# Kernel tuning notes

Hardware: AMD Instinct MI355X
Metric: run time of the kernel (lower is better)

## Reference

```python
import jax, jax.numpy as jnp
import numpy as np
from jax import lax

NPOINT = 1024
RADIUS = 0.2
NSAMPLE = 32
BN_EPS = 1e-5
MLP = [64, 64, 128]


def setup_inputs() -> dict:
    key = jax.random.key(0)
    ks = jax.random.split(key, 2 + 3 * len(MLP))
    B, N, D = 16, 4096, 64
    inp = {
        "xyz": jax.random.uniform(ks[0], (B, N, 3), dtype=jnp.float32),
        "points": jax.random.normal(ks[1], (B, N, D), dtype=jnp.float32),
    }
    last = 3 + D  # in_channel = 67
    for i, oc in enumerate(MLP):
        inp[f"w{i}"] = jax.random.normal(ks[2 + 3 * i], (oc, last), dtype=jnp.float32) / np.sqrt(last).astype(np.float32)
        inp[f"b{i}"] = jnp.zeros((oc,), jnp.float32)
        inp[f"g{i}"] = jnp.ones((oc,), jnp.float32)
        inp[f"bt{i}"] = jnp.zeros((oc,), jnp.float32)
        last = oc
    return inp


def _sqrdist(a, b):
    # ||a-b||^2 = |a|^2 + |b|^2 - 2 a.b   -> [B, S, N], avoids [B,S,N,3] temp
    return (jnp.sum(a * a, -1)[:, :, None]
            + jnp.sum(b * b, -1)[:, None, :]
            - 2.0 * jnp.einsum('bsc,bnc->bsn', a, b))


def _fps(xyz, npoint):
    # Farthest point sampling; deterministic start at index 0 per batch.
    B, N, _ = xyz.shape

    def step(carry, _):
        distance, far = carry
        centroid = jnp.take_along_axis(xyz, far[:, None, None], axis=1)  # [B,1,3]
        d = jnp.sum((xyz - centroid) ** 2, -1)                           # [B,N]
        distance = jnp.minimum(distance, d)
        nxt = jnp.argmax(distance, -1).astype(jnp.int32)
        return (distance, nxt), far

    init = (jnp.full((B, N), 1e10, xyz.dtype), jnp.zeros((B,), jnp.int32))
    _, idx = lax.scan(step, init, None, length=npoint)
    return jnp.transpose(idx)  # [B, npoint]


def _ball_query(radius, nsample, xyz, new_xyz):
    B, N, _ = xyz.shape
    sq = _sqrdist(new_xyz, xyz)                                          # [B,S,N]
    gid = jnp.where(sq > radius ** 2, N, jnp.arange(N, dtype=jnp.int32)[None, None, :])
    gid = jnp.sort(gid, axis=-1)[:, :, :nsample]                         # [B,S,K]
    first = gid[:, :, :1]
    return jnp.where(gid == N, first, gid)


def _gather(points, idx):
    # points [B,N,C], idx [B,...] -> [B,...,C]
    return jax.vmap(lambda p, i: p[i])(points, idx)


def reference(xyz, points, w0, b0, g0, bt0, w1, b1, g1, bt1, w2, b2, g2, bt2):
    B, N, _ = xyz.shape
    fps_idx = _fps(xyz, NPOINT)                                          # [B,S]
    new_xyz = _gather(xyz, fps_idx)                                      # [B,S,3]
    idx = _ball_query(RADIUS, NSAMPLE, xyz, new_xyz)                     # [B,S,K]
    grouped_xyz = _gather(xyz, idx)                                      # [B,S,K,3]
    grouped_xyz_norm = grouped_xyz - new_xyz[:, :, None, :]
    grouped_pts = _gather(points, idx)                                   # [B,S,K,D]
    x = jnp.concatenate([grouped_xyz_norm, grouped_pts], axis=-1)        # [B,S,K,3+D]

    # pointwise (1x1 conv) MLP with training-mode BatchNorm + ReLU
    for w, b, g, bt in ((w0, b0, g0, bt0), (w1, b1, g1, bt1), (w2, b2, g2, bt2)):
        x = jnp.einsum('bskc,oc->bsko', x, w) + b
        mean = jnp.mean(x, axis=(0, 1, 2))
        var = jnp.var(x, axis=(0, 1, 2))
        x = jax.nn.relu(g * (x - mean) * lax.rsqrt(var + BN_EPS) + bt)

    new_points = jnp.max(x, axis=2)                                      # [B,S,Cout]
    return new_xyz, new_points
```

## Files before the change

### kernel.cpp

```cpp
#include <hip/hip_runtime.h>
#include <stdint.h>

#define B_ 16
#define N_ 4096
#define D_ 64
#define S_ 1024
#define K_ 32
#define M_ (B_*S_*K_)
#define NQ_ (B_*S_)
#define EPS_ 1e-5f
#define WPAD 72
#define FCH 256

typedef short bf16x8 __attribute__((ext_vector_type(8)));
typedef float f32x4  __attribute__((ext_vector_type(4)));
typedef float f32x2  __attribute__((ext_vector_type(2)));

struct F3 { float x, y, z; };

static __device__ __forceinline__ float bf2f(uint16_t u){
  union{uint32_t i; float f;} v; v.i = ((uint32_t)u) << 16; return v.f;
}
static __device__ __forceinline__ uint16_t f2bf(float f){
  union{uint32_t i; float f;} v; v.f = f;
  uint32_t u = v.i;
  uint32_t r = (u + 0x7FFFu + ((u >> 16) & 1u)) >> 16;
  return (uint16_t)r;
}

#define DPP_MAXSTEP(k, CTRL) {                                                   \
  unsigned _lo = (unsigned)(k), _hi = (unsigned)((k) >> 32);                     \
  unsigned _plo = (unsigned)__builtin_amdgcn_update_dpp((int)_lo, (int)_lo,      \
                                                        CTRL, 0xf, 0xf, false); \
  unsigned _phi = (unsigned)__builtin_amdgcn_update_dpp((int)_hi, (int)_hi,      \
                                                        CTRL, 0xf, 0xf, false); \
  unsigned long long _pk = ((unsigned long long)_phi << 32) | _plo;              \
  if(_pk > (k)) (k) = _pk; }

static __device__ __forceinline__ bf16x8 h1_frag(const uint16_t* __restrict__ y1t,
                                                 const float* la0s, const float* lb0s,
                                                 int m, int kb){
  const uint32_t* __restrict__ y32 = (const uint32_t*)y1t;
  const int c2 = kb >> 1;
  uint32_t wrd[4];
#pragma unroll
  for(int i = 0; i < 4; ++i) wrd[i] = y32[(size_t)(c2 + i) * M_ + m];
  bf16x8 f;
#pragma unroll
  for(int i = 0; i < 4; ++i){
    int c0 = kb + 2*i;
    float v0 = bf2f((uint16_t)(wrd[i] & 0xFFFFu));
    float v1 = bf2f((uint16_t)(wrd[i] >> 16));
    float h0 = fmaxf(la0s[c0]   * v0 + lb0s[c0],   0.0f);
    float h1 = fmaxf(la0s[c0+1] * v1 + lb0s[c0+1], 0.0f);
    f[2*i]   = (short)f2bf(h0);
    f[2*i+1] = (short)f2bf(h1);
  }
  return f;
}

__global__ __launch_bounds__(256)
void fps_chunk_kernel(const float* __restrict__ xyz,
                      float* __restrict__ out_newxyz,
                      f32x2* __restrict__ dstate,
                      int* __restrict__ farws,
                      int it0, int itend, int is_first, int is_last){
  const int b = blockIdx.x;
  const int tid = threadIdx.x;
  const float* X = xyz + (size_t)b * N_ * 3;
  __shared__ float4 sxyz[N_];
  __shared__ __align__(16) unsigned long long slots[2][4];
  __shared__ float outbuf[FCH * 3];
  f32x2 px[8], py[8], pz[8], dist[8];
#pragma unroll
  for(int j = 0; j < 8; ++j){
    int p0 = tid + (2*j)   * 256;
    int p1 = tid + (2*j+1) * 256;
    px[j].x = X[p0*3 + 0]; px[j].y = X[p1*3 + 0];
    py[j].x = X[p0*3 + 1]; py[j].y = X[p1*3 + 1];
    pz[j].x = X[p0*3 + 2]; pz[j].y = X[p1*3 + 2];
    sxyz[p0] = make_float4(px[j].x, py[j].x, pz[j].x, 0.0f);
    sxyz[p1] = make_float4(px[j].y, py[j].y, pz[j].y, 0.0f);
  }
  if(is_first){
#pragma unroll
    for(int j = 0; j < 8; ++j){ dist[j].x = 1e10f; dist[j].y = 1e10f; }
  } else {
#pragma unroll
    for(int j = 0; j < 8; ++j) dist[j] = dstate[((size_t)b*8 + j)*256 + tid];
  }
  int far = is_first ? 0 : farws[b];
  __syncthreads();
  for(int it = it0; it < itend; ++it){
    float4 c = sxyz[far];
    if(tid == 0){
      int lo = (it - it0) * 3;
      outbuf[lo + 0] = c.x; outbuf[lo + 1] = c.y; outbuf[lo + 2] = c.z;
    }
    if(it == S_ - 1) break;
    f32x2 cx; cx.x = c.x; cx.y = c.x;
    f32x2 cy; cy.x = c.y; cy.y = c.y;
    f32x2 cz; cz.x = c.z; cz.y = c.z;
    float bestd = -1.0f; int bestt = 0;
#pragma unroll
    for(int j = 0; j < 8; ++j){
      f32x2 nd;
      {
#pragma clang fp contract(off)
        f32x2 dx = px[j] - cx, dy = py[j] - cy, dz = pz[j] - cz;
        f32x2 d  = dx*dx + dy*dy + dz*dz;
        nd = __builtin_elementwise_min(dist[j], d);
      }
      dist[j] = nd;
      if(nd.x > bestd){ bestd = nd.x; bestt = 2*j; }
      if(nd.y > bestd){ bestd = nd.y; bestt = 2*j+1; }
    }
    const int bestp = tid + (bestt << 8);
    unsigned long long key = ((unsigned long long)__float_as_uint(bestd) << 32)
                           | (unsigned long long)(uint32_t)(~bestp);
    DPP_MAXSTEP(key, 0x111);
    DPP_MAXSTEP(key, 0x112);
    DPP_MAXSTEP(key, 0x114);
    DPP_MAXSTEP(key, 0x118);
    DPP_MAXSTEP(key, 0x142);
    DPP_MAXSTEP(key, 0x143);
    const int par = it & 1;
    if((tid & 63) == 63) slots[par][tid >> 6] = key;
    __syncthreads();
    ulonglong2 s01 = *(const ulonglong2*)&slots[par][0];
    ulonglong2 s23 = *(const ulonglong2*)&slots[par][2];
    unsigned long long bk = s01.x;
    if(s01.y > bk) bk = s01.y;
    if(s23.x > bk) bk = s23.x;
    if(s23.y > bk) bk = s23.y;
    far = (int)(~(uint32_t)bk);
  }
  if(!is_last){
#pragma unroll
    for(int j = 0; j < 8; ++j) dstate[((size_t)b*8 + j)*256 + tid] = dist[j];
    if(tid == 0) farws[b] = far;
  }
  __syncthreads();
  float* O = out_newxyz + (size_t)b * S_ * 3 + (size_t)it0 * 3;
  const int cnt = (itend - it0) * 3;
  for(int i = tid; i < cnt; i += 256) O[i] = outbuf[i];
}

__global__ __launch_bounds__(256) void ballq_kernel(const float* __restrict__ xyz,
                                                    const float* __restrict__ newxyz,
                                                    int* __restrict__ gidx,
                                                    float* __restrict__ gstats){
  const int tid = threadIdx.x;
  if(blockIdx.x == 0){
    gstats[tid] = 0.0f; gstats[256 + tid] = 0.0f;
  }
  const int wslot = tid >> 6;
  const int lane  = tid & 63;
  const int q = blockIdx.x * 4 + wslot;
  const int b = q >> 10;
  const F3* XP = (const F3*)(xyz + (size_t)b * N_ * 3);
  const double R2D = 0.2 * 0.2;
  float nxf, nyf, nzf, saf;
  double nx, ny, nz, sa;
  {
    const float* NP = newxyz + (size_t)q * 3;
    nxf = NP[0]; nyf = NP[1]; nzf = NP[2];
    saf = nxf*nxf + nyf*nyf + nzf*nzf;
    nx = (double)nxf; ny = (double)nyf; nz = (double)nzf;
    sa = nx*nx + ny*ny + nz*nz;
  }
  __shared__ int sidx[4][K_];
  int count = 0;
  for(int base = 0; base < N_; base += 64){
    int p = base + lane;
    F3 pt = XP[p];
    float sb32 = pt.x*pt.x + pt.y*pt.y + pt.z*pt.z;
    float dt32 = nxf*pt.x + nyf*pt.y + nzf*pt.z;
    float sq32 = saf + sb32 - 2.0f * dt32;
    bool band = fabsf(sq32 - 0.04f) < 5e-5f;
    bool inb;
    if(__ballot(band) != 0ull){
      double pxv = (double)pt.x, pyv = (double)pt.y, pzv = (double)pt.z;
      double sb = pxv*pxv + pyv*pyv + pzv*pzv;
      double dt = nx*pxv + ny*pyv + nz*pzv;
      double sq = sa + sb - 2.0 * dt;
      inb = !(sq > R2D);
    } else {
      inb = !(sq32 > 0.04f);
    }
    unsigned long long mask = __ballot(inb);
    int pos = count + __popcll(mask & ((1ull << lane) - 1ull));
    if(inb && pos < K_) sidx[wslot][pos] = p;
    count += (int)__popcll(mask);
    if(count >= K_) break;
  }
  __syncthreads();
  int nvalid = count < K_ ? count : K_;
  if(lane < K_){
    int first = sidx[wslot][0];
    int v = (lane < nvalid) ? sidx[wslot][lane] : first;
    gidx[(size_t)q * K_ + lane] = v;
  }
}

__global__ __launch_bounds__(256)
void layer1_kernel(const float* __restrict__ xyz,
                   const float* __restrict__ pts,
                   const float* __restrict__ newxyz,
                   const int* __restrict__ gidx,
                   const float* __restrict__ w,
                   const float* __restrict__ bias,
                   uint16_t* __restrict__ y1t,
                   float* __restrict__ gstats){
  __shared__ float xT[67*128];
  __shared__ float wT[67*64];
  __shared__ float sm_sum[64], sm_sq[64];
  const int tid = threadIdx.x;
  const int bm = blockIdx.x * 128;

  for(int i = tid; i < 67*64; i += 256){
    int o = i / 67, c = i - o*67;
    wT[c*64 + o] = w[i];
  }
  {
    const int r = tid >> 1, h = tid & 1;
    const int m = bm + r;
    const int bs = m >> 5, b = bs >> 10;
    const int j = gidx[m];
    const float4* pr = (const float4*)(pts + ((size_t)b * N_ + j) * D_);
    if(h == 0){
      const float* nxp = newxyz + (size_t)bs * 3;
      const float* pp  = xyz + ((size_t)b * N_ + j) * 3;
      xT[0*128 + r] = pp[0] - nxp[0];
      xT[1*128 + r] = pp[1] - nxp[1];
      xT[2*128 + r] = pp[2] - nxp[2];
#pragma unroll
      for(int k = 0; k < 8; ++k){
        float4 v = pr[k];
        xT[(3 + 4*k + 0)*128 + r] = v.x; xT[(3 + 4*k + 1)*128 + r] = v.y;
        xT[(3 + 4*k + 2)*128 + r] = v.z; xT[(3 + 4*k + 3)*128 + r] = v.w;
      }
    } else {
#pragma unroll
      for(int k = 8; k < 16; ++k){
        float4 v = pr[k];
        xT[(3 + 4*k + 0)*128 + r] = v.x; xT[(3 + 4*k + 1)*128 + r] = v.y;
        xT[(3 + 4*k + 2)*128 + r] = v.z; xT[(3 + 4*k + 3)*128 + r] = v.w;
      }
    }
  }
  __syncthreads();

  const int mq = tid & 15;
  const int oq = tid >> 4;
  float acc[8][4];
  {
    float4 bv = *(const float4*)&bias[oq*4];
#pragma unroll
    for(int mi = 0; mi < 8; ++mi){
      acc[mi][0] = bv.x; acc[mi][1] = bv.y; acc[mi][2] = bv.z; acc[mi][3] = bv.w;
    }
  }
  for(int c = 0; c < 67; ++c){
    f32x4 xa = *(const f32x4*)&xT[c*128 + mq*8];
    f32x4 xb = *(const f32x4*)&xT[c*128 + mq*8 + 4];
    f32x4 wv = *(const f32x4*)&wT[c*64 + oq*4];
#pragma unroll
    for(int mi = 0; mi < 4; ++mi){
      float xv = xa[mi];
#pragma unroll
      for(int oi = 0; oi < 4; ++oi) acc[mi][oi] = fmaf(wv[oi], xv, acc[mi][oi]);
    }
#pragma unroll
    for(int mi = 4; mi < 8; ++mi){
      float xv = xb[mi-4];
#pragma unroll
      for(int oi = 0; oi < 4; ++oi) acc[mi][oi] = fmaf(wv[oi], xv, acc[mi][oi]);
    }
  }

  {
    float s[4], q[4];
#pragma unroll
    for(int oi = 0; oi < 4; ++oi){
      float ss = 0.f, qq = 0.f;
#pragma unroll
      for(int mi = 0; mi < 8; ++mi){
        ss += acc[mi][oi]; qq = fmaf(acc[mi][oi], acc[mi][oi], qq);
      }
      s[oi] = ss; q[oi] = qq;
    }
#pragma unroll
    for(int d = 1; d < 16; d <<= 1){
#pragma unroll
      for(int oi = 0; oi < 4; ++oi){
        s[oi] += __shfl_xor(s[oi], d, 64);
        q[oi] += __shfl_xor(q[oi], d, 64);
      }
    }
    if(mq == 0){
#pragma unroll
      for(int oi = 0; oi < 4; ++oi){
        sm_sum[oq*4 + oi] = s[oi];
        sm_sq [oq*4 + oi] = q[oi];
      }
    }
  }

  {
    uint32_t* __restrict__ y1o = (uint32_t*)y1t;
#pragma unroll
    for(int p = 0; p < 2; ++p){
      uint32_t pk[8];
#pragma unroll
      for(int mi = 0; mi < 8; ++mi){
        uint32_t lo = (uint32_t)f2bf(acc[mi][2*p]);
        uint32_t hi = (uint32_t)f2bf(acc[mi][2*p + 1]);
        pk[mi] = lo | (hi << 16);
      }
      uint32_t* dst = &y1o[(size_t)(oq*2 + p) * M_ + bm + mq*8];
      *(uint4*)(dst)     = make_uint4(pk[0], pk[1], pk[2], pk[3]);
      *(uint4*)(dst + 4) = make_uint4(pk[4], pk[5], pk[6], pk[7]);
    }
  }
  __syncthreads();
  if(tid < 64)       atomicAdd(&gstats[tid],      sm_sum[tid]);
  else if(tid < 128) atomicAdd(&gstats[tid],      sm_sq[tid - 64]);
}

__global__ __launch_bounds__(256)
void layer2_stats_kernel(const uint16_t* __restrict__ y1t,
                         const float* __restrict__ gstats0,
                         const float* __restrict__ g0,
                         const float* __restrict__ bt0,
                         const float* __restrict__ w1,
                         const float* __restrict__ b1,
                         float* __restrict__ gstats1){
  __shared__ short w1b[64*WPAD];
  __shared__ float la0s[64], lb0s[64], b1s[64];
  __shared__ float ssum[64], ssq[64];
  const int tid = threadIdx.x;
#pragma unroll
  for(int i = 0; i < 16; ++i){
    int e = i*256 + tid;
    w1b[(e>>6)*WPAD + (e&63)] = (short)f2bf(w1[e]);
  }
  if(tid < 64){
    float mean = gstats0[tid] * (1.0f / M_);
    float var  = gstats0[64 + tid] * (1.0f / M_) - mean * mean;
    float inv  = 1.0f / sqrtf(var + EPS_);
    float a = g0[tid] * inv;
    la0s[tid] = a; lb0s[tid] = bt0[tid] - mean * a;
    b1s[tid] = b1[tid];
  } else if(tid < 128){
    ssum[tid-64] = 0.f; ssq[tid-64] = 0.f;
  }
  __syncthreads();

  const int wave = tid >> 6, lane = tid & 63;
  const int row = lane & 15, quad = lane >> 4;

  for(int ck = 0; ck < 4; ++ck){
    const int wm0 = blockIdx.x * 512 + ck * 128 + wave * 32;
    bf16x8 afr[2][2];
#pragma unroll
    for(int s = 0; s < 2; ++s)
#pragma unroll
      for(int k2 = 0; k2 < 2; ++k2)
        afr[s][k2] = h1_frag(y1t, la0s, lb0s, wm0 + s*16 + row, quad*8 + k2*32);

    for(int ot = 0; ot < 4; ++ot){
      bf16x8 bfr0 = *(const bf16x8*)&w1b[(ot*16 + row)*WPAD + quad*8];
      bf16x8 bfr1 = *(const bf16x8*)&w1b[(ot*16 + row)*WPAD + quad*8 + 32];
      const float bb = b1s[ot*16 + row];
      float sum_ = 0.f, sq_ = 0.f;
#pragma unroll
      for(int s = 0; s < 2; ++s){
        f32x4 acc = {0.f, 0.f, 0.f, 0.f};
        acc = __builtin_amdgcn_mfma_f32_16x16x32_bf16(afr[s][0], bfr0, acc, 0, 0, 0);
        acc = __builtin_amdgcn_mfma_f32_16x16x32_bf16(afr[s][1], bfr1, acc, 0, 0, 0);
#pragma unroll
        for(int r = 0; r < 4; ++r){
          float z = acc[r] + bb;
          sum_ += z; sq_ = fmaf(z, z, sq_);
        }
      }
      sum_ += __shfl_xor(sum_, 16, 64); sum_ += __shfl_xor(sum_, 32, 64);
      sq_  += __shfl_xor(sq_,  16, 64); sq_  += __shfl_xor(sq_,  32, 64);
      if(quad == 0){
        atomicAdd(&ssum[ot*16 + row], sum_);
        atomicAdd(&ssq [ot*16 + row], sq_);
      }
    }
  }
  __syncthreads();
  if(tid < 64)       atomicAdd(&gstats1[tid], ssum[tid]);
  else if(tid < 128) atomicAdd(&gstats1[tid], ssq[tid - 64]);
}

__global__ __launch_bounds__(256)
void layer3_kernel(const uint16_t* __restrict__ y1t,
                   const float* __restrict__ gstats0,
                   const float* __restrict__ g0,
                   const float* __restrict__ bt0,
                   const float* __restrict__ w1,
                   const float* __restrict__ b1,
                   const float* __restrict__ gstats1,
                   const float* __restrict__ g1,
                   const float* __restrict__ bt1,
                   const float* __restrict__ w2,
                   const float* __restrict__ b2,
                   float* __restrict__ gstats2,
                   float* __restrict__ maxk,
                   float* __restrict__ mink){
  __shared__ short w1b[64*WPAD];
  __shared__ short w2b[128*WPAD];
  __shared__ short h2s[4][32*WPAD];
  __shared__ float la0s[64], lb0s[64], la1s[64], lb1s[64], b1s[64], b2s[128];
  __shared__ float ssum[128], ssq[128];
  const int tid = threadIdx.x;
#pragma unroll
  for(int i = 0; i < 16; ++i){
    int e = i*256 + tid;
    w1b[(e>>6)*WPAD + (e&63)] = (short)f2bf(w1[e]);
  }
#pragma unroll
  for(int i = 0; i < 32; ++i){
    int e = i*256 + tid;
    w2b[(e>>6)*WPAD + (e&63)] = (short)f2bf(w2[e]);
  }
  if(tid < 64){
    float mean = gstats0[tid] * (1.0f / M_);
    float var  = gstats0[64 + tid] * (1.0f / M_) - mean * mean;
    float inv  = 1.0f / sqrtf(var + EPS_);
    float a = g0[tid] * inv;
    la0s[tid] = a; lb0s[tid] = bt0[tid] - mean * a;
    b1s[tid] = b1[tid];
  } else if(tid < 128){
    int o = tid - 64;
    float mean = gstats1[o] * (1.0f / M_);
    float var  = gstats1[64 + o] * (1.0f / M_) - mean * mean;
    float inv  = 1.0f / sqrtf(var + EPS_);
    float a = g1[o] * inv;
    la1s[o] = a; lb1s[o] = bt1[o] - mean * a;
  }
  if(tid < 128){ b2s[tid] = b2[tid]; ssum[tid] = 0.f; }
  else         { ssq[tid - 128] = 0.f; }
  __syncthreads();

  const int wave = tid >> 6, lane = tid & 63;
  const int row = lane & 15, quad = lane >> 4;
  short* h2w = &h2s[wave][0];

  for(int ck = 0; ck < 4; ++ck){
    const int wm0 = blockIdx.x * 512 + ck * 128 + wave * 32;
    {
      bf16x8 afr[2][2];
#pragma unroll
      for(int s = 0; s < 2; ++s)
#pragma unroll
        for(int k2 = 0; k2 < 2; ++k2)
          afr[s][k2] = h1_frag(y1t, la0s, lb0s, wm0 + s*16 + row, quad*8 + k2*32);

      for(int ot = 0; ot < 4; ++ot){
        bf16x8 bfr0 = *(const bf16x8*)&w1b[(ot*16 + row)*WPAD + quad*8];
        bf16x8 bfr1 = *(const bf16x8*)&w1b[(ot*16 + row)*WPAD + quad*8 + 32];
        const int o = ot*16 + row;
        const float bb = b1s[o], a1 = la1s[o], c1 = lb1s[o];
#pragma unroll
        for(int s = 0; s < 2; ++s){
          f32x4 acc = {0.f, 0.f, 0.f, 0.f};
          acc = __builtin_amdgcn_mfma_f32_16x16x32_bf16(afr[s][0], bfr0, acc, 0, 0, 0);
          acc = __builtin_amdgcn_mfma_f32_16x16x32_bf16(afr[s][1], bfr1, acc, 0, 0, 0);
#pragma unroll
          for(int r = 0; r < 4; ++r){
            float z = acc[r] + bb;
            float h = fmaxf(a1 * z + c1, 0.0f);
            int ml = s*16 + quad*4 + r;
            h2w[ml*WPAD + o] = (short)f2bf(h);
          }
        }
      }
    }
    {
      bf16x8 hfr[2][2];
#pragma unroll
      for(int s = 0; s < 2; ++s)
#pragma unroll
        for(int k2 = 0; k2 < 2; ++k2)
          hfr[s][k2] = *(const bf16x8*)&h2w[(s*16 + row)*WPAD + quad*8 + k2*32];

      for(int ot = 0; ot < 8; ++ot){
        bf16x8 bfr0 = *(const bf16x8*)&w2b[(ot*16 + row)*WPAD + quad*8];
        bf16x8 bfr1 = *(const bf16x8*)&w2b[(ot*16 + row)*WPAD + quad*8 + 32];
        const int o = ot*16 + row;
        const float bb = b2s[o];
        float sum_ = 0.f, sq_ = 0.f, mx = -1e30f, mn = 1e30f;
#pragma unroll
        for(int s = 0; s < 2; ++s){
          f32x4 acc = {0.f, 0.f, 0.f, 0.f};
          acc = __builtin_amdgcn_mfma_f32_16x16x32_bf16(hfr[s][0], bfr0, acc, 0, 0, 0);
          acc = __builtin_amdgcn_mfma_f32_16x16x32_bf16(hfr[s][1], bfr1, acc, 0, 0, 0);
#pragma unroll
          for(int r = 0; r < 4; ++r){
            float z = acc[r] + bb;
            sum_ += z; sq_ = fmaf(z, z, sq_);
            mx = fmaxf(mx, z); mn = fminf(mn, z);
          }
        }
        sum_ += __shfl_xor(sum_, 16, 64); sum_ += __shfl_xor(sum_, 32, 64);
        sq_  += __shfl_xor(sq_,  16, 64); sq_  += __shfl_xor(sq_,  32, 64);
        mx = fmaxf(mx, __shfl_xor(mx, 16, 64)); mx = fmaxf(mx, __shfl_xor(mx, 32, 64));
        mn = fminf(mn, __shfl_xor(mn, 16, 64)); mn = fminf(mn, __shfl_xor(mn, 32, 64));
        if(quad == 0){
          atomicAdd(&ssum[o], sum_);
          atomicAdd(&ssq [o], sq_);
          maxk[(size_t)(wm0 >> 5) * 128 + o] = mx;
          mink[(size_t)(wm0 >> 5) * 128 + o] = mn;
        }
      }
    }
  }
  __syncthreads();
  if(tid < 128) atomicAdd(&gstats2[tid], ssum[tid]);
  else          atomicAdd(&gstats2[tid], ssq[tid - 128]);
}

__global__ __launch_bounds__(256) void final_kernel(const float* __restrict__ maxk,
                                                    const float* __restrict__ mink,
                                                    const float* __restrict__ gstats2,
                                                    const float* __restrict__ g,
                                                    const float* __restrict__ bt,
                                                    float* __restrict__ out_np){
  const int gid = blockIdx.x * 256 + threadIdx.x;
  const int o = gid & 127;
  float mean = gstats2[o] * (1.0f / M_);
  float var  = gstats2[128 + o] * (1.0f / M_) - mean * mean;
  float inv  = 1.0f / sqrtf(var + EPS_);
  float a = g[o] * inv;
  float b = bt[o] - mean * a;
  float mx = maxk[gid], mn = mink[gid];
  out_np[gid] = fmaxf(fmaxf(a * mx + b, 0.0f), fmaxf(a * mn + b, 0.0f));
}

extern "C" void kernel_launch(void* const* d_in, const int* in_sizes, int n_in,
                              void* d_out, int out_size, void* d_ws, size_t ws_size,
                              hipStream_t stream){
  (void)in_sizes; (void)n_in; (void)out_size;
  const float* xyz = (const float*)d_in[0];
  const float* pts = (const float*)d_in[1];
  const float* w0 = (const float*)d_in[2];  const float* b0  = (const float*)d_in[3];
  const float* g0 = (const float*)d_in[4];  const float* bt0 = (const float*)d_in[5];
  const float* w1 = (const float*)d_in[6];  const float* b1  = (const float*)d_in[7];
  const float* g1 = (const float*)d_in[8];  const float* bt1 = (const float*)d_in[9];
  const float* w2 = (const float*)d_in[10]; const float* b2  = (const float*)d_in[11];
  const float* g2 = (const float*)d_in[12]; const float* bt2 = (const float*)d_in[13];

  float* out    = (float*)d_out;
  float* newxyz = out;
  float* newpts = out + (size_t)B_ * S_ * 3;

  const size_t off_gidx  = 0;
  const size_t off_stats = off_gidx  + (size_t)M_ * 4;
  const size_t off_maxk  = off_stats + 65536;
  const size_t off_mink  = off_maxk  + (size_t)NQ_ * 128 * 4;
  const size_t off_y1    = off_mink  + (size_t)NQ_ * 128 * 4;
  const size_t off_fd    = off_y1    + (size_t)M_ * 64 * 2;
  const size_t off_ff    = off_fd    + (size_t)B_ * 8 * 256 * 8;
  const size_t need      = off_ff    + 256;
  if(ws_size < need) return;

  char* ws = (char*)d_ws;
  int*      gidx   = (int*)     (ws + off_gidx);
  float*    gstats = (float*)   (ws + off_stats);
  float*    maxk   = (float*)   (ws + off_maxk);
  float*    mink   = (float*)   (ws + off_mink);
  uint16_t* y1t    = (uint16_t*)(ws + off_y1);
  f32x2*    dstate = (f32x2*)   (ws + off_fd);
  int*      farws  = (int*)     (ws + off_ff);

  for(int k = 0; k < 4; ++k){
    fps_chunk_kernel<<<B_, 256, 0, stream>>>(xyz, newxyz, dstate, farws,
                                             k*FCH, (k+1)*FCH,
                                             k == 0 ? 1 : 0, k == 3 ? 1 : 0);
  }
  ballq_kernel<<<NQ_ / 4, 256, 0, stream>>>(xyz, newxyz, gidx, gstats);

  layer1_kernel      <<<M_ / 128, 256, 0, stream>>>(xyz, pts, newxyz, gidx, w0, b0, y1t, gstats);
  layer2_stats_kernel<<<M_ / 512, 256, 0, stream>>>(y1t, gstats, g0, bt0, w1, b1, gstats + 128);
  layer3_kernel      <<<M_ / 512, 256, 0, stream>>>(y1t, gstats, g0, bt0, w1, b1,
                                                    gstats + 128, g1, bt1, w2, b2,
                                                    gstats + 256, maxk, mink);
  final_kernel<<<(NQ_ * 128) / 256, 256, 0, stream>>>(maxk, mink, gstats + 256, g2, bt2, newpts);
}
```

Before: 970.7 us.

## Overlap FPS chunks with ball query and layer1 via fused staged launches

Merges the FPS chunk, ball-query and layer-1 kernels into one kernel whose role is chosen by block index. Each launch runs the next FPS chunk while ball query works on the previous chunk's centroids and layer 1 works on the chunk before that, so the serial FPS (16 blocks) overlaps with the parallel work. The cost is a 67 KB shared-memory footprint for every block, which limits occupancy of the ball-query and layer-1 roles, plus a longer pipeline of six launches.

After: 919.5 us. 5.3% less time.

```diff
diff --git a/kernel.cpp b/kernel.cpp
--- a/kernel.cpp
+++ b/kernel.cpp
@@ -11,6 +11,8 @@
 #define EPS_ 1e-5f
 #define WPAD 72
 #define FCH 256
+#define NBQ_ 1024
+#define NL1_ 1024
 
 typedef short bf16x8 __attribute__((ext_vector_type(8)));
 typedef float f32x4  __attribute__((ext_vector_type(4)));
@@ -60,272 +62,276 @@
 }
 
 __global__ __launch_bounds__(256)
-void fps_chunk_kernel(const float* __restrict__ xyz,
-                      float* __restrict__ out_newxyz,
-                      f32x2* __restrict__ dstate,
-                      int* __restrict__ farws,
-                      int it0, int itend, int is_first, int is_last){
-  const int b = blockIdx.x;
+void fused_kernel(const float* __restrict__ xyz,
+                  const float* __restrict__ pts,
+                  float* __restrict__ out_newxyz,
+                  f32x2* __restrict__ dstate,
+                  int* __restrict__ farws,
+                  int* __restrict__ gidx,
+                  float* __restrict__ gstats,
+                  const float* __restrict__ w,
+                  const float* __restrict__ bias,
+                  uint16_t* __restrict__ y1t,
+                  int nfps, int it0, int itend, int is_first, int is_last,
+                  int nbq, int bq_qoff, int bq_zero,
+                  int l1_qoff){
+  __shared__ __align__(16) char smem[68672];
+  const int bid = blockIdx.x;
   const int tid = threadIdx.x;
-  const float* X = xyz + (size_t)b * N_ * 3;
-  __shared__ float4 sxyz[N_];
-  __shared__ __align__(16) unsigned long long slots[2][4];
-  __shared__ float outbuf[FCH * 3];
-  f32x2 px[8], py[8], pz[8], dist[8];
-#pragma unroll
-  for(int j = 0; j < 8; ++j){
-    int p0 = tid + (2*j)   * 256;
-    int p1 = tid + (2*j+1) * 256;
-    px[j].x = X[p0*3 + 0]; px[j].y = X[p1*3 + 0];
-    py[j].x = X[p0*3 + 1]; py[j].y = X[p1*3 + 1];
-    pz[j].x = X[p0*3 + 2]; pz[j].y = X[p1*3 + 2];
-    sxyz[p0] = make_float4(px[j].x, py[j].x, pz[j].x, 0.0f);
-    sxyz[p1] = make_float4(px[j].y, py[j].y, pz[j].y, 0.0f);
-  }
-  if(is_first){
-#pragma unroll
-    for(int j = 0; j < 8; ++j){ dist[j].x = 1e10f; dist[j].y = 1e10f; }
+
+  if(bid < nfps){
+    const int b = bid;
+    const float* X = xyz + (size_t)b * N_ * 3;
+    float4* sxyz = (float4*)smem;
+    unsigned long long* slots = (unsigned long long*)(smem + 65536);
+    float* outbuf = (float*)(smem + 65600);
+    f32x2 px[8], py[8], pz[8], dist[8];
+#pragma unroll
+    for(int j = 0; j < 8; ++j){
+      int p0 = tid + (2*j)   * 256;
+      int p1 = tid + (2*j+1) * 256;
+      px[j].x = X[p0*3 + 0]; px[j].y = X[p1*3 + 0];
+      py[j].x = X[p0*3 + 1]; py[j].y = X[p1*3 + 1];
+      pz[j].x = X[p0*3 + 2]; pz[j].y = X[p1*3 + 2];
+      sxyz[p0] = make_float4(px[j].x, py[j].x, pz[j].x, 0.0f);
+      sxyz[p1] = make_float4(px[j].y, py[j].y, pz[j].y, 0.0f);
+    }
+    if(is_first){
+#pragma unroll
+      for(int j = 0; j < 8; ++j){ dist[j].x = 1e10f; dist[j].y = 1e10f; }
+    } else {
+#pragma unroll
+      for(int j = 0; j < 8; ++j) dist[j] = dstate[((size_t)b*8 + j)*256 + tid];
+    }
+    int far = is_first ? 0 : farws[b];
+    __syncthreads();
+    for(int it = it0; it < itend; ++it){
+      float4 c = sxyz[far];
+      if(tid == 0){
+        int lo = (it - it0) * 3;
+        outbuf[lo + 0] = c.x; outbuf[lo + 1] = c.y; outbuf[lo + 2] = c.z;
+      }
+      if(it == S_ - 1) break;
+      f32x2 cx; cx.x = c.x; cx.y = c.x;
+      f32x2 cy; cy.x = c.y; cy.y = c.y;
+      f32x2 cz; cz.x = c.z; cz.y = c.z;
+      float bestd = -1.0f; int bestt = 0;
+#pragma unroll
+      for(int j = 0; j < 8; ++j){
+        f32x2 nd;
+        {
+#pragma clang fp contract(off)
+          f32x2 dx = px[j] - cx, dy = py[j] - cy, dz = pz[j] - cz;
+          f32x2 d  = dx*dx + dy*dy + dz*dz;
+          nd = __builtin_elementwise_min(dist[j], d);
+        }
+        dist[j] = nd;
+        if(nd.x > bestd){ bestd = nd.x; bestt = 2*j; }
+        if(nd.y > bestd){ bestd = nd.y; bestt = 2*j+1; }
+      }
+      const int bestp = tid + (bestt << 8);
+      unsigned long long key = ((unsigned long long)__float_as_uint(bestd) << 32)
+                             | (unsigned long long)(uint32_t)(~bestp);
+      DPP_MAXSTEP(key, 0x111);
+      DPP_MAXSTEP(key, 0x112);
+      DPP_MAXSTEP(key, 0x114);
+      DPP_MAXSTEP(key, 0x118);
+      DPP_MAXSTEP(key, 0x142);
+      DPP_MAXSTEP(key, 0x143);
+      const int par = it & 1;
+      if((tid & 63) == 63) slots[par*4 + (tid >> 6)] = key;
+      __syncthreads();
+      ulonglong2 s01 = *(const ulonglong2*)&slots[par*4];
+      ulonglong2 s23 = *(const ulonglong2*)&slots[par*4 + 2];
+      unsigned long long bk = s01.x;
+      if(s01.y > bk) bk = s01.y;
+      if(s23.x > bk) bk = s23.x;
+      if(s23.y > bk) bk = s23.y;
+      far = (int)(~(uint32_t)bk);
+    }
+    if(!is_last){
+#pragma unroll
+      for(int j = 0; j < 8; ++j) dstate[((size_t)b*8 + j)*256 + tid] = dist[j];
+      if(tid == 0) farws[b] = far;
+    }
+    __syncthreads();
+    float* O = out_newxyz + (size_t)b * S_ * 3 + (size_t)it0 * 3;
+    const int cnt = (itend - it0) * 3;
+    for(int i = tid; i < cnt; i += 256) O[i] = outbuf[i];
+
+  } else if(bid < nfps + nbq){
+    const int local = bid - nfps;
+    int* sidx = (int*)smem;
+    if(bq_zero && local == 0){
+      gstats[tid] = 0.0f; gstats[256 + tid] = 0.0f;
+    }
+    const int wslot = tid >> 6;
+    const int lane  = tid & 63;
+    const int t = local * 4 + wslot;
+    const int q = ((t >> 8) << 10) + bq_qoff + (t & 255);
+    const int b = q >> 10;
+    const F3* XP = (const F3*)(xyz + (size_t)b * N_ * 3);
+    const double R2D = 0.2 * 0.2;
+    float nxf, nyf, nzf, saf;
+    double nx, ny, nz, sa;
+    {
+      const float* NP = out_newxyz + (size_t)q * 3;
+      nxf = NP[0]; nyf = NP[1]; nzf = NP[2];
+      saf = nxf*nxf + nyf*nyf + nzf*nzf;
+      nx = (double)nxf; ny = (double)nyf; nz = (double)nzf;
+      sa = nx*nx + ny*ny + nz*nz;
+    }
+    int count = 0;
+    for(int base = 0; base < N_; base += 64){
+      int p = base + lane;
+      F3 pt = XP[p];
+      float sb32 = pt.x*pt.x + pt.y*pt.y + pt.z*pt.z;
+      float dt32 = nxf*pt.x + nyf*pt.y + nzf*pt.z;
+      float sq32 = saf + sb32 - 2.0f * dt32;
+      bool band = fabsf(sq32 - 0.04f) < 5e-5f;
+      bool inb;
+      if(__ballot(band) != 0ull){
+        double pxv = (double)pt.x, pyv = (double)pt.y, pzv = (double)pt.z;
+        double sb = pxv*pxv + pyv*pyv + pzv*pzv;
+        double dt = nx*pxv + ny*pyv + nz*pzv;
+        double sq = sa + sb - 2.0 * dt;
+        inb = !(sq > R2D);
+      } else {
+        inb = !(sq32 > 0.04f);
+      }
+      unsigned long long mask = __ballot(inb);
+      int pos = count + __popcll(mask & ((1ull << lane) - 1ull));
+      if(inb && pos < K_) sidx[wslot*K_ + pos] = p;
+      count += (int)__popcll(mask);
+      if(count >= K_) break;
+    }
+    __syncthreads();
+    int nvalid = count < K_ ? count : K_;
+    if(lane < K_){
+      int first = sidx[wslot*K_ + 0];
+      int v = (lane < nvalid) ? sidx[wslot*K_ + lane] : first;
+      gidx[(size_t)q * K_ + lane] = v;
+    }
+
   } else {
-#pragma unroll
-    for(int j = 0; j < 8; ++j) dist[j] = dstate[((size_t)b*8 + j)*256 + tid];
-  }
-  int far = is_first ? 0 : farws[b];
-  __syncthreads();
-  for(int it = it0; it < itend; ++it){
-    float4 c = sxyz[far];
-    if(tid == 0){
-      int lo = (it - it0) * 3;
-      outbuf[lo + 0] = c.x; outbuf[lo + 1] = c.y; outbuf[lo + 2] = c.z;
-    }
-    if(it == S_ - 1) break;
-    f32x2 cx; cx.x = c.x; cx.y = c.x;
-    f32x2 cy; cy.x = c.y; cy.y = c.y;
-    f32x2 cz; cz.x = c.z; cz.y = c.z;
-    float bestd = -1.0f; int bestt = 0;
-#pragma unroll
-    for(int j = 0; j < 8; ++j){
-      f32x2 nd;
-      {
-#pragma clang fp contract(off)
-        f32x2 dx = px[j] - cx, dy = py[j] - cy, dz = pz[j] - cz;
-        f32x2 d  = dx*dx + dy*dy + dz*dz;
-        nd = __builtin_elementwise_min(dist[j], d);
-      }
-      dist[j] = nd;
-      if(nd.x > bestd){ bestd = nd.x; bestt = 2*j; }
-      if(nd.y > bestd){ bestd = nd.y; bestt = 2*j+1; }
-    }
-    const int bestp = tid + (bestt << 8);
-    unsigned long long key = ((unsigned long long)__float_as_uint(bestd) << 32)
-                           | (unsigned long long)(uint32_t)(~bestp);
-    DPP_MAXSTEP(key, 0x111);
-    DPP_MAXSTEP(key, 0x112);
-    DPP_MAXSTEP(key, 0x114);
-    DPP_MAXSTEP(key, 0x118);
-    DPP_MAXSTEP(key, 0x142);
-    DPP_MAXSTEP(key, 0x143);
-    const int par = it & 1;
-    if((tid & 63) == 63) slots[par][tid >> 6] = key;
+    const int local = bid - nfps - nbq;
+    float* xT     = (float*)smem;
+    float* wT     = (float*)(smem + 34304);
+    float* sm_sum = (float*)(smem + 51456);
+    float* sm_sq  = (float*)(smem + 51712);
+    const int tq = local * 4;
+    const int q0 = ((tq >> 8) << 10) + l1_qoff + (tq & 255);
+    const int bm = q0 * 32;
+
+    for(int i = tid; i < 67*64; i += 256){
+      int o = i / 67, c = i - o*67;
+      wT[c*64 + o] = w[i];
+    }
+    {
+      const int r = tid >> 1, h = tid & 1;
+      const int m = bm + r;
+      const int bs = m >> 5, b = bs >> 10;
+      const int j = gidx[m];
+      const float4* pr = (const float4*)(pts + ((size_t)b * N_ + j) * D_);
+      if(h == 0){
+        const float* nxp = out_newxyz + (size_t)bs * 3;
+        const float* pp  = xyz + ((size_t)b * N_ + j) * 3;
+        xT[0*128 + r] = pp[0] - nxp[0];
+        xT[1*128 + r] = pp[1] - nxp[1];
+        xT[2*128 + r] = pp[2] - nxp[2];
+#pragma unroll
+        for(int k = 0; k < 8; ++k){
+          float4 v = pr[k];
+          xT[(3 + 4*k + 0)*128 + r] = v.x; xT[(3 + 4*k + 1)*128 + r] = v.y;
+          xT[(3 + 4*k + 2)*128 + r] = v.z; xT[(3 + 4*k + 3)*128 + r] = v.w;
+        }
+      } else {
+#pragma unroll
+        for(int k = 8; k < 16; ++k){
+          float4 v = pr[k];
+          xT[(3 + 4*k + 0)*128 + r] = v.x; xT[(3 + 4*k + 1)*128 + r] = v.y;
+          xT[(3 + 4*k + 2)*128 + r] = v.z; xT[(3 + 4*k + 3)*128 + r] = v.w;
+        }
+      }
+    }
     __syncthreads();
-    ulonglong2 s01 = *(const ulonglong2*)&slots[par][0];
-    ulonglong2 s23 = *(const ulonglong2*)&slots[par][2];
-    unsigned long long bk = s01.x;
-    if(s01.y > bk) bk = s01.y;
-    if(s23.x > bk) bk = s23.x;
-    if(s23.y > bk) bk = s23.y;
-    far = (int)(~(uint32_t)bk);
-  }
-  if(!is_last){
-#pragma unroll
-    for(int j = 0; j < 8; ++j) dstate[((size_t)b*8 + j)*256 + tid] = dist[j];
-    if(tid == 0) farws[b] = far;
-  }
-  __syncthreads();
-  float* O = out_newxyz + (size_t)b * S_ * 3 + (size_t)it0 * 3;
-  const int cnt = (itend - it0) * 3;
-  for(int i = tid; i < cnt; i += 256) O[i] = outbuf[i];
-}
-
-__global__ __launch_bounds__(256) void ballq_kernel(const float* __restrict__ xyz,
-                                                    const float* __restrict__ newxyz,
-                                                    int* __restrict__ gidx,
-                                                    float* __restrict__ gstats){
-  const int tid = threadIdx.x;
-  if(blockIdx.x == 0){
-    gstats[tid] = 0.0f; gstats[256 + tid] = 0.0f;
-  }
-  const int wslot = tid >> 6;
-  const int lane  = tid & 63;
-  const int q = blockIdx.x * 4 + wslot;
-  const int b = q >> 10;
-  const F3* XP = (const F3*)(xyz + (size_t)b * N_ * 3);
-  const double R2D = 0.2 * 0.2;
-  float nxf, nyf, nzf, saf;
-  double nx, ny, nz, sa;
-  {
-    const float* NP = newxyz + (size_t)q * 3;
-    nxf = NP[0]; nyf = NP[1]; nzf = NP[2];
-    saf = nxf*nxf + nyf*nyf + nzf*nzf;
-    nx = (double)nxf; ny = (double)nyf; nz = (double)nzf;
-    sa = nx*nx + ny*ny + nz*nz;
-  }
-  __shared__ int sidx[4][K_];
-  int count = 0;
-  for(int base = 0; base < N_; base += 64){
-    int p = base + lane;
-    F3 pt = XP[p];
-    float sb32 = pt.x*pt.x + pt.y*pt.y + pt.z*pt.z;
-    float dt32 = nxf*pt.x + nyf*pt.y + nzf*pt.z;
-    float sq32 = saf + sb32 - 2.0f * dt32;
-    bool band = fabsf(sq32 - 0.04f) < 5e-5f;
-    bool inb;
-    if(__ballot(band) != 0ull){
-      double pxv = (double)pt.x, pyv = (double)pt.y, pzv = (double)pt.z;
-      double sb = pxv*pxv + pyv*pyv + pzv*pzv;
-      double dt = nx*pxv + ny*pyv + nz*pzv;
-      double sq = sa + sb - 2.0 * dt;
-      inb = !(sq > R2D);
-    } else {
-      inb = !(sq32 > 0.04f);
-    }
-    unsigned long long mask = __ballot(inb);
-    int pos = count + __popcll(mask & ((1ull << lane) - 1ull));
-    if(inb && pos < K_) sidx[wslot][pos] = p;
-    count += (int)__popcll(mask);
-    if(count >= K_) break;
-  }
-  __syncthreads();
-  int nvalid = count < K_ ? count : K_;
-  if(lane < K_){
-    int first = sidx[wslot][0];
-    int v = (lane < nvalid) ? sidx[wslot][lane] : first;
-    gidx[(size_t)q * K_ + lane] = v;
-  }
-}
-
-__global__ __launch_bounds__(256)
-void layer1_kernel(const float* __restrict__ xyz,
-                   const float* __restrict__ pts,
-                   const float* __restrict__ newxyz,
-                   const int* __restrict__ gidx,
-                   const float* __restrict__ w,
-                   const float* __restrict__ bias,
-                   uint16_t* __restrict__ y1t,
-                   float* __restrict__ gstats){
-  __shared__ float xT[67*128];
-  __shared__ float wT[67*64];
-  __shared__ float sm_sum[64], sm_sq[64];
-  const int tid = threadIdx.x;
-  const int bm = blockIdx.x * 128;
-
-  for(int i = tid; i < 67*64; i += 256){
-    int o = i / 67, c = i - o*67;
-    wT[c*64 + o] = w[i];
-  }
-  {
-    const int r = tid >> 1, h = tid & 1;
-    const int m = bm + r;
-    const int bs = m >> 5, b = bs >> 10;
-    const int j = gidx[m];
-    const float4* pr = (const float4*)(pts + ((size_t)b * N_ + j) * D_);
-    if(h == 0){
-      const float* nxp = newxyz + (size_t)bs * 3;
-      const float* pp  = xyz + ((size_t)b * N_ + j) * 3;
-      xT[0*128 + r] = pp[0] - nxp[0];
-      xT[1*128 + r] = pp[1] - nxp[1];
-      xT[2*128 + r] = pp[2] - nxp[2];
-#pragma unroll
-      for(int k = 0; k < 8; ++k){
-        float4 v = pr[k];
-        xT[(3 + 4*k + 0)*128 + r] = v.x; xT[(3 + 4*k + 1)*128 + r] = v.y;
-        xT[(3 + 4*k + 2)*128 + r] = v.z; xT[(3 + 4*k + 3)*128 + r] = v.w;
-      }
-    } else {
-#pragma unroll
-      for(int k = 8; k < 16; ++k){
-        float4 v = pr[k];
-        xT[(3 + 4*k + 0)*128 + r] = v.x; xT[(3 + 4*k + 1)*128 + r] = v.y;
-        xT[(3 + 4*k + 2)*128 + r] = v.z; xT[(3 + 4*k + 3)*128 + r] = v.w;
-      }
-    }
-  }
-  __syncthreads();
-
-  const int mq = tid & 15;
-  const int oq = tid >> 4;
-  float acc[8][4];
-  {
-    float4 bv = *(const float4*)&bias[oq*4];
-#pragma unroll
-    for(int mi = 0; mi < 8; ++mi){
-      acc[mi][0] = bv.x; acc[mi][1] = bv.y; acc[mi][2] = bv.z; acc[mi][3] = bv.w;
-    }
-  }
-  for(int c = 0; c < 67; ++c){
-    f32x4 xa = *(const f32x4*)&xT[c*128 + mq*8];
-    f32x4 xb = *(const f32x4*)&xT[c*128 + mq*8 + 4];
-    f32x4 wv = *(const f32x4*)&wT[c*64 + oq*4];
-#pragma unroll
-    for(int mi = 0; mi < 4; ++mi){
-      float xv = xa[mi];
-#pragma unroll
-      for(int oi = 0; oi < 4; ++oi) acc[mi][oi] = fmaf(wv[oi], xv, acc[mi][oi]);
-    }
-#pragma unroll
-    for(int mi = 4; mi < 8; ++mi){
-      float xv = xb[mi-4];
-#pragma unroll
-      for(int oi = 0; oi < 4; ++oi) acc[mi][oi] = fmaf(wv[oi], xv, acc[mi][oi]);
-    }
-  }
-
-  {
-    float s[4], q[4];
-#pragma unroll
-    for(int oi = 0; oi < 4; ++oi){
-      float ss = 0.f, qq = 0.f;
+
+    const int mq = tid & 15;
+    const int oq = tid >> 4;
+    float acc[8][4];
+    {
+      float4 bv = *(const float4*)&bias[oq*4];
 #pragma unroll
       for(int mi = 0; mi < 8; ++mi){
-        ss += acc[mi][oi]; qq = fmaf(acc[mi][oi], acc[mi][oi], qq);
-      }
-      s[oi] = ss; q[oi] = qq;
-    }
-#pragma unroll
-    for(int d = 1; d < 16; d <<= 1){
+        acc[mi][0] = bv.x; acc[mi][1] = bv.y; acc[mi][2] = bv.z; acc[mi][3] = bv.w;
+      }
+    }
+    for(int c = 0; c < 67; ++c){
+      f32x4 xa = *(const f32x4*)&xT[c*128 + mq*8];
+      f32x4 xb = *(const f32x4*)&xT[c*128 + mq*8 + 4];
+      f32x4 wv = *(const f32x4*)&wT[c*64 + oq*4];
+#pragma unroll
+      for(int mi = 0; mi < 4; ++mi){
+        float xv = xa[mi];
+#pragma unroll
+        for(int oi = 0; oi < 4; ++oi) acc[mi][oi] = fmaf(wv[oi], xv, acc[mi][oi]);
+      }
+#pragma unroll
+      for(int mi = 4; mi < 8; ++mi){
+        float xv = xb[mi-4];
+#pragma unroll
+        for(int oi = 0; oi < 4; ++oi) acc[mi][oi] = fmaf(wv[oi], xv, acc[mi][oi]);
+      }
+    }
+
+    {
+      float s[4], qv[4];
 #pragma unroll
       for(int oi = 0; oi < 4; ++oi){
-        s[oi] += __shfl_xor(s[oi], d, 64);
-        q[oi] += __shfl_xor(q[oi], d, 64);
-      }
-    }
-    if(mq == 0){
-#pragma unroll
-      for(int oi = 0; oi < 4; ++oi){
-        sm_sum[oq*4 + oi] = s[oi];
-        sm_sq [oq*4 + oi] = q[oi];
-      }
-    }
-  }
-
-  {
-    uint32_t* __restrict__ y1o = (uint32_t*)y1t;
-#pragma unroll
-    for(int p = 0; p < 2; ++p){
-      uint32_t pk[8];
-#pragma unroll
-      for(int mi = 0; mi < 8; ++mi){
-        uint32_t lo = (uint32_t)f2bf(acc[mi][2*p]);
-        uint32_t hi = (uint32_t)f2bf(acc[mi][2*p + 1]);
-        pk[mi] = lo | (hi << 16);
-      }
-      uint32_t* dst = &y1o[(size_t)(oq*2 + p) * M_ + bm + mq*8];
-      *(uint4*)(dst)     = make_uint4(pk[0], pk[1], pk[2], pk[3]);
-      *(uint4*)(dst + 4) = make_uint4(pk[4], pk[5], pk[6], pk[7]);
-    }
-  }
-  __syncthreads();
-  if(tid < 64)       atomicAdd(&gstats[tid],      sm_sum[tid]);
-  else if(tid < 128) atomicAdd(&gstats[tid],      sm_sq[tid - 64]);
+        float ss = 0.f, qq = 0.f;
+#pragma unroll
+        for(int mi = 0; mi < 8; ++mi){
+          ss += acc[mi][oi]; qq = fmaf(acc[mi][oi], acc[mi][oi], qq);
+        }
+        s[oi] = ss; qv[oi] = qq;
+      }
+#pragma unroll
+      for(int d = 1; d < 16; d <<= 1){
+#pragma unroll
+        for(int oi = 0; oi < 4; ++oi){
+          s[oi]  += __shfl_xor(s[oi],  d, 64);
+          qv[oi] += __shfl_xor(qv[oi], d, 64);
+        }
+      }
+      if(mq == 0){
+#pragma unroll
+        for(int oi = 0; oi < 4; ++oi){
+          sm_sum[oq*4 + oi] = s[oi];
+          sm_sq [oq*4 + oi] = qv[oi];
+        }
+      }
+    }
+
+    {
+      uint32_t* __restrict__ y1o = (uint32_t*)y1t;
+#pragma unroll
+      for(int p = 0; p < 2; ++p){
+        uint32_t pk[8];
+#pragma unroll
+        for(int mi = 0; mi < 8; ++mi){
+          uint32_t lo = (uint32_t)f2bf(acc[mi][2*p]);
+          uint32_t hi = (uint32_t)f2bf(acc[mi][2*p + 1]);
+          pk[mi] = lo | (hi << 16);
+        }
+        uint32_t* dst = &y1o[(size_t)(oq*2 + p) * M_ + bm + mq*8];
+        *(uint4*)(dst)     = make_uint4(pk[0], pk[1], pk[2], pk[3]);
+        *(uint4*)(dst + 4) = make_uint4(pk[4], pk[5], pk[6], pk[7]);
+      }
+    }
+    __syncthreads();
+    if(tid < 64)       atomicAdd(&gstats[tid],      sm_sum[tid]);
+    else if(tid < 128) atomicAdd(&gstats[tid],      sm_sq[tid - 64]);
+  }
 }
 
 __global__ __launch_bounds__(256)
@@ -579,14 +585,31 @@
   f32x2*    dstate = (f32x2*)   (ws + off_fd);
   int*      farws  = (int*)     (ws + off_ff);
 
-  for(int k = 0; k < 4; ++k){
-    fps_chunk_kernel<<<B_, 256, 0, stream>>>(xyz, newxyz, dstate, farws,
-                                             k*FCH, (k+1)*FCH,
-                                             k == 0 ? 1 : 0, k == 3 ? 1 : 0);
-  }
-  ballq_kernel<<<NQ_ / 4, 256, 0, stream>>>(xyz, newxyz, gidx, gstats);
-
-  layer1_kernel      <<<M_ / 128, 256, 0, stream>>>(xyz, pts, newxyz, gidx, w0, b0, y1t, gstats);
+  fused_kernel<<<16, 256, 0, stream>>>(xyz, pts, newxyz, dstate, farws,
+                                       gidx, gstats, w0, b0, y1t,
+                                       16, 0*FCH, 1*FCH, 1, 0,
+                                       0, 0, 0,   0);
+  fused_kernel<<<16 + NBQ_, 256, 0, stream>>>(xyz, pts, newxyz, dstate, farws,
+                                       gidx, gstats, w0, b0, y1t,
+                                       16, 1*FCH, 2*FCH, 0, 0,
+                                       NBQ_, 0, 1,   0);
+  fused_kernel<<<16 + NBQ_ + NL1_, 256, 0, stream>>>(xyz, pts, newxyz, dstate, farws,
+                                       gidx, gstats, w0, b0, y1t,
+                                       16, 2*FCH, 3*FCH, 0, 0,
+                                       NBQ_, 256, 0,   0);
+  fused_kernel<<<16 + NBQ_ + NL1_, 256, 0, stream>>>(xyz, pts, newxyz, dstate, farws,
+                                       gidx, gstats, w0, b0, y1t,
+                                       16, 3*FCH, 4*FCH, 0, 1,
+                                       NBQ_, 512, 0,   256);
+  fused_kernel<<<NBQ_ + NL1_, 256, 0, stream>>>(xyz, pts, newxyz, dstate, farws,
+                                       gidx, gstats, w0, b0, y1t,
+                                       0, 0, 0, 0, 0,
+                                       NBQ_, 768, 0,   512);
+  fused_kernel<<<NL1_, 256, 0, stream>>>(xyz, pts, newxyz, dstate, farws,
+                                       gidx, gstats, w0, b0, y1t,
+                                       0, 0, 0, 0, 0,
+                                       0, 0, 0,   768);
+
   layer2_stats_kernel<<<M_ / 512, 256, 0, stream>>>(y1t, gstats, g0, bt0, w1, b1, gstats + 128);
   layer3_kernel      <<<M_ / 512, 256, 0, stream>>>(y1t, gstats, g0, bt0, w1, b1,
                                                     gstats + 128, g1, bt1, w2, b2,
```
